# Kernel optimization log

Hardware: AMD Instinct MI355X
Metric: run time of the kernel (lower is better)

## Reference

```python
import jax, jax.numpy as jnp
import numpy as np

B, S, D, H, C = 8, 4096, 1024, 256, 512
INIT_RANGE = 0.01

def setup_inputs() -> dict:
    key = jax.random.key(0)
    ks = jax.random.split(key, 6)
    return {
        "hidden_states": jax.random.normal(ks[0], (B, S, D), dtype=jnp.float32),
        "conditions": jax.random.normal(ks[1], (B, C), dtype=jnp.float32),
        "down_project": jax.random.normal(ks[2], (D, H), dtype=jnp.float32) * INIT_RANGE,
        "down_gamma": jax.random.normal(ks[3], (C, H), dtype=jnp.float32),
        "down_beta": jnp.zeros((C, H), dtype=jnp.float32),
        "up_project": jax.random.normal(ks[4], (H, D), dtype=jnp.float32) * INIT_RANGE,
        "up_gamma": jax.random.normal(ks[5], (C, D), dtype=jnp.float32),
        "up_beta": jnp.zeros((C, D), dtype=jnp.float32),
    }

def reference(hidden_states, conditions, down_project, down_gamma, down_beta,
              up_project, up_gamma, up_beta):
    # per-example modulation coefficients: [B, H] / [B, D]
    dg = conditions @ down_gamma   # [B, H]
    db = conditions @ down_beta    # [B, H]
    ug = conditions @ up_gamma     # [B, D]
    ub = conditions @ up_beta      # [B, D]
    # per-example down weight: W_down * gamma (column scale) + beta (added to every row)
    w_down = down_project[None, :, :] * dg[:, None, :] + db[:, None, :]  # [B, D, H]
    down = jnp.einsum('bsd,bdh->bsh', hidden_states, w_down)             # [B, S, H]
    act = jax.nn.relu(down)
    w_up = up_project[None, :, :] * ug[:, None, :] + ub[:, None, :]      # [B, H, D]
    up = jnp.einsum('bsh,bhd->bsd', act, w_up)                           # [B, S, D]
    # (the original computes self.ln(up) but discards the result)
    return up + hidden_states
```

## Files before the change

### kernel.cpp

```cpp
#include <hip/hip_runtime.h>
#include <hip/hip_bf16.h>

typedef __attribute__((ext_vector_type(4))) float f32x4;
typedef __attribute__((ext_vector_type(8))) short s16x8;
typedef __attribute__((ext_vector_type(8))) unsigned short u16x8;
typedef __attribute__((ext_vector_type(4))) unsigned int u32x4;

#define DEVFN static __device__ __forceinline__

DEVFN unsigned short f2bf(float f) {
  union { float f; unsigned int u; } v; v.f = f;
  unsigned int u = v.u;
  u += 0x7fffu + ((u >> 16) & 1u);
  return (unsigned short)(u >> 16);
}

DEVFN unsigned int cvt_pk(float a, float b) {
  __hip_bfloat162 h = __float22bfloat162_rn(make_float2(a, b));
  union { __hip_bfloat162 h; unsigned int u; } v; v.h = h; return v.u;
}

DEVFN void gl_lds16(const void* g, void* l) {
  __builtin_amdgcn_global_load_lds((__attribute__((address_space(1))) void*)g,
                                   (__attribute__((address_space(3))) void*)l, 16, 0, 0);
}

#define SB() __builtin_amdgcn_sched_barrier(0)
#define VMW(n) asm volatile("s_waitcnt vmcnt(" #n ")" ::: "memory")
#define LGKM0() asm volatile("s_waitcnt lgkmcnt(0)" ::: "memory")
#define BAR() { SB(); __builtin_amdgcn_s_barrier(); SB(); }

#define DG_OFF 0
#define DB_OFF 2048
#define UG_OFF 4096
#define UB_OFF 12288
#define W1_BYTE 81920
#define W2_BYTE 606208

__global__ void prep_kernel(const float* __restrict__ cond,
                            const float* __restrict__ dgm, const float* __restrict__ dbt,
                            const float* __restrict__ ugm, const float* __restrict__ ubt,
                            const float* __restrict__ Wd, const float* __restrict__ Wu,
                            char* __restrict__ ws) {
  __shared__ float lc[4096];
  __shared__ float red[2048];
  const int t = threadIdx.x;

  if (blockIdx.x < 32) {
    const int ks = blockIdx.x;
    const int n = t;
    const float* sp = Wd + (size_t)(ks * 32) * 256 + n;
    unsigned short tmp[32];
#pragma unroll
    for (int kk = 0; kk < 32; ++kk) tmp[kk] = f2bf(sp[(size_t)kk * 256]);
    char* dst = ws + W1_BYTE + (size_t)ks * 16384 + n * 64;
#pragma unroll
    for (int g = 0; g < 4; ++g) {
      u16x8 v;
#pragma unroll
      for (int e = 0; e < 8; ++e) v[e] = tmp[g * 8 + e];
      *(u16x8*)(dst + ((g ^ ((n >> 1) & 3)) << 4)) = v;
    }
    return;
  }
  if (blockIdx.x < 64) {
    int b2 = blockIdx.x - 32;
    int ntile = b2 >> 2, kc = b2 & 3;
    const int n = t >> 1, kh = t & 1;
    const float* sp = Wu + (size_t)(kc * 64 + kh * 32) * 1024 + ntile * 128 + n;
    unsigned short tmp[32];
#pragma unroll
    for (int kk = 0; kk < 32; ++kk) tmp[kk] = f2bf(sp[(size_t)kk * 1024]);
    char* dst = ws + W2_BYTE + (size_t)(ntile * 4 + kc) * 16384 + n * 128;
#pragma unroll
    for (int gi = 0; gi < 4; ++gi) {
      u16x8 v;
#pragma unroll
      for (int e = 0; e < 8; ++e) v[e] = tmp[gi * 8 + e];
      int g = kh * 4 + gi;
      *(u16x8*)(dst + ((g ^ (n & 7)) << 4)) = v;
    }
    return;
  }

  float* coef = (float*)ws;
#pragma unroll
  for (int i = 0; i < 16; ++i) lc[t + i * 256] = cond[t + i * 256];
  __syncthreads();
  const int bid2 = blockIdx.x - 64;
  const int col = bid2 * 16 + (t & 15);
  const int ks = t >> 4;
  const float* src; int ncol, cl;
  if (col < 256)       { src = dgm; ncol = 256;  cl = col; }
  else if (col < 512)  { src = dbt; ncol = 256;  cl = col - 256; }
  else if (col < 1536) { src = ugm; ncol = 1024; cl = col - 512; }
  else                 { src = ubt; ncol = 1024; cl = col - 1536; }
  float acc[8] = {};
  for (int k = ks * 32; k < ks * 32 + 32; ++k) {
    float g = src[(size_t)k * ncol + cl];
#pragma unroll
    for (int b = 0; b < 8; ++b) acc[b] = fmaf(lc[b * 512 + k], g, acc[b]);
  }
#pragma unroll
  for (int b = 0; b < 8; ++b) red[(ks * 16 + (t & 15)) * 8 + b] = acc[b];
  __syncthreads();
  if (t < 128) {
    int c = t >> 3, b = t & 7;
    float s = 0.f;
#pragma unroll
    for (int k2 = 0; k2 < 16; ++k2) s += red[(k2 * 16 + c) * 8 + b];
    int colg = bid2 * 16 + c;
    float* dst; int ncol2, cl2;
    if (colg < 256)       { dst = coef + DG_OFF; ncol2 = 256;  cl2 = colg; }
    else if (colg < 512)  { dst = coef + DB_OFF; ncol2 = 256;  cl2 = colg - 256; }
    else if (colg < 1536) { dst = coef + UG_OFF; ncol2 = 1024; cl2 = colg - 512; }
    else                  { dst = coef + UB_OFF; ncol2 = 1024; cl2 = colg - 1536; }
    dst[b * ncol2 + cl2] = s;
  }
}

__global__ __launch_bounds__(512, 4)
void fused_kernel(const float* __restrict__ X, char* __restrict__ ws,
                  float* __restrict__ out) {
  __shared__ char lds[81920];
  const int tid = threadIdx.x;
  const int lane = tid & 63, lr = lane & 15, lq = lane >> 4;
  const int wave = tid >> 6;
  const int wm = wave >> 2, wn = wave & 3;

  const int raw = blockIdx.x;
  const int m = (raw & 7) * 64 + (raw >> 3);
  const int row0 = m << 6;
  const int b = m >> 6;

  const float* coef = (const float*)ws;
  const char* w1 = ws + W1_BYTE;
  const char* w2 = ws + W2_BYTE;

  const int srow = tid >> 4, sg = tid & 15;
  const float* xsrc = X + (size_t)(row0 + srow) * 1024 + ((sg ^ (srow & 15)) << 2);

  int aoff[2][2][2];
#pragma unroll
  for (int mf = 0; mf < 2; ++mf)
#pragma unroll
    for (int h = 0; h < 2; ++h) {
      int r = wm * 32 + mf * 16 + lr;
      int g0 = h * 8 + lq * 2;
      aoff[mf][h][0] = r * 256 + ((g0 ^ (r & 15)) << 4);
      aoff[mf][h][1] = r * 256 + (((g0 + 1) ^ (r & 15)) << 4);
    }
  int boff[4];
#pragma unroll
  for (int nf = 0; nf < 4; ++nf) {
    int n = wn * 64 + nf * 16 + lr;
    boff[nf] = n * 64 + ((lq ^ ((n >> 1) & 3)) << 4);
  }

  f32x4 acc1[2][4] = {};
  float hacc[2] = {0.f, 0.f};

#define STAGE_X(t)                                                               \
  { char* xb = lds + ((t) & 1) * 16384;                                          \
    gl_lds16(xsrc + (size_t)(t) * 64, xb + tid * 16);                            \
    gl_lds16(xsrc + 32 * 1024 + (size_t)(t) * 64, xb + 8192 + tid * 16); }
#define STAGE_W1(ks)                                                             \
  { char* dst = lds + 32768 + ((ks) % 3) * 16384;                                \
    gl_lds16(w1 + (size_t)(ks) * 16384 + tid * 16, dst + tid * 16);              \
    gl_lds16(w1 + (size_t)(ks) * 16384 + 8192 + tid * 16, dst + 8192 + tid * 16); }

  STAGE_W1(0); STAGE_X(0); STAGE_W1(1);
  VMW(2); BAR();

#pragma unroll
  for (int s = 0; s < 32; ++s) {
    if (s + 2 < 32) STAGE_W1(s + 2);
    if ((s & 1) == 0 && (s >> 1) + 1 < 16) STAGE_X((s >> 1) + 1);
    {
      const char* Xc = lds + ((s >> 1) & 1) * 16384;
      const char* Wb = lds + 32768 + (s % 3) * 16384;
      const int h = s & 1;
      s16x8 afr[2];
#pragma unroll
      for (int mf = 0; mf < 2; ++mf) {
        f32x4 fa0 = *(const f32x4*)(Xc + aoff[mf][h][0]);
        f32x4 fa1 = *(const f32x4*)(Xc + aoff[mf][h][1]);
        if (wn == 0)
          hacc[mf] += fa0[0] + fa0[1] + fa0[2] + fa0[3] +
                      fa1[0] + fa1[1] + fa1[2] + fa1[3];
        union { u32x4 u; s16x8 s_; } cv;
        cv.u[0] = cvt_pk(fa0[0], fa0[1]); cv.u[1] = cvt_pk(fa0[2], fa0[3]);
        cv.u[2] = cvt_pk(fa1[0], fa1[1]); cv.u[3] = cvt_pk(fa1[2], fa1[3]);
        afr[mf] = cv.s_;
      }
      s16x8 bfr[4];
#pragma unroll
      for (int nf = 0; nf < 4; ++nf) bfr[nf] = *(const s16x8*)(Wb + boff[nf]);
#pragma unroll
      for (int mf = 0; mf < 2; ++mf)
#pragma unroll
        for (int nf = 0; nf < 4; ++nf)
          acc1[mf][nf] = __builtin_amdgcn_mfma_f32_16x16x32_bf16(afr[mf], bfr[nf],
                                                                 acc1[mf][nf], 0, 0, 0);
    }
    LGKM0(); SB();
    if (s == 30)            { VMW(0); }
    else if (s == 31)       { }
    else if (s & 1)         { VMW(2); }
    else                    { VMW(4); }
    BAR();
  }

  float* hsumb = (float*)(lds + 32768);
  float* asp   = (float*)(lds + 33024);
  if (wn == 0) {
#pragma unroll
    for (int mf = 0; mf < 2; ++mf) {
      float s = hacc[mf];
      s += __shfl_xor(s, 16); s += __shfl_xor(s, 32);
      if (lq == 0) hsumb[wm * 32 + mf * 16 + lr] = s;
    }
  }
  __syncthreads();

  float dgv[4], dbv[4];
#pragma unroll
  for (int nf = 0; nf < 4; ++nf) {
    int h = wn * 64 + nf * 16 + lr;
    dgv[nf] = coef[DG_OFF + b * 256 + h];
    dbv[nf] = coef[DB_OFF + b * 256 + h];
  }

  float asacc[2][4] = {};
#pragma unroll
  for (int nf = 0; nf < 4; ++nf) {
    int g = nf * 2 + (lr >> 3);
    char* nbase = lds + wn * 8192 + (lr & 7) * 2;
    float dg_ = dgv[nf], db_ = dbv[nf];
#pragma unroll
    for (int mf = 0; mf < 2; ++mf) {
#pragma unroll
      for (int j = 0; j < 4; ++j) {
        int r = wm * 32 + mf * 16 + lq * 4 + j;
        float v = acc1[mf][nf][j] * dg_ + db_ * hsumb[r];
        v = fmaxf(v, 0.f);
        asacc[mf][j] += v;
        *(unsigned short*)(nbase + r * 128 + ((g ^ (r & 7)) << 4)) = f2bf(v);
      }
    }
  }
#pragma unroll
  for (int mf = 0; mf < 2; ++mf)
#pragma unroll
    for (int j = 0; j < 4; ++j) {
      float s = asacc[mf][j];
      s += __shfl_xor(s, 1); s += __shfl_xor(s, 2); s += __shfl_xor(s, 4); s += __shfl_xor(s, 8);
      if (lr == 0) asp[wn * 64 + wm * 32 + mf * 16 + lq * 4 + j] = s;
    }
  __syncthreads();

  float asv[2][4];
#pragma unroll
  for (int mf = 0; mf < 2; ++mf)
#pragma unroll
    for (int j = 0; j < 4; ++j) {
      int r = wm * 32 + mf * 16 + lq * 4 + j;
      asv[mf][j] = asp[r] + asp[64 + r] + asp[128 + r] + asp[192 + r];
    }
  __syncthreads();

  int a2off[2][2], b2off[2][2];
#pragma unroll
  for (int mf = 0; mf < 2; ++mf)
#pragma unroll
    for (int kf = 0; kf < 2; ++kf) {
      int r = wm * 32 + mf * 16 + lr;
      a2off[mf][kf] = r * 128 + (((kf * 4 + lq) ^ (r & 7)) << 4);
    }
#pragma unroll
  for (int nf = 0; nf < 2; ++nf)
#pragma unroll
    for (int kf = 0; kf < 2; ++kf) {
      int nl = wn * 32 + nf * 16 + lr;
      b2off[nf][kf] = nl * 128 + (((kf * 4 + lq) ^ (nl & 7)) << 4);
    }

#define W2B(s) (lds + 32768 + ((s) % 3) * 16384)
#define STAGE_W2(s)                                                              \
  { gl_lds16(w2 + (size_t)(s) * 16384 + tid * 16, W2B(s) + tid * 16);            \
    gl_lds16(w2 + (size_t)(s) * 16384 + 8192 + tid * 16,                         \
             W2B(s) + 8192 + tid * 16); }

  STAGE_W2(0); STAGE_W2(1);
  VMW(2); BAR();

  float ugv[2], ubv[2];
#pragma unroll
  for (int s = 0; s < 32; ++s) {
    const int nt = s >> 2, kc = s & 3;
    f32x4 acc2[2][2];
    if (kc == 0) {
#pragma unroll
      for (int mf = 0; mf < 2; ++mf)
#pragma unroll
        for (int nf = 0; nf < 2; ++nf) acc2[mf][nf] = (f32x4){0.f, 0.f, 0.f, 0.f};
    }
    const char* Wb = W2B(s);
#pragma unroll
    for (int kf = 0; kf < 2; ++kf) {
      s16x8 a2[2], bb[2];
#pragma unroll
      for (int mf = 0; mf < 2; ++mf)
        a2[mf] = *(const s16x8*)(lds + kc * 8192 + a2off[mf][kf]);
#pragma unroll
      for (int nf = 0; nf < 2; ++nf)
        bb[nf] = *(const s16x8*)(Wb + b2off[nf][kf]);
#pragma unroll
      for (int mf = 0; mf < 2; ++mf)
#pragma unroll
        for (int nf = 0; nf < 2; ++nf)
          acc2[mf][nf] = __builtin_amdgcn_mfma_f32_16x16x32_bf16(a2[mf], bb[nf], acc2[mf][nf], 0, 0, 0);
    }
    LGKM0(); SB();

    if (kc == 0) {
#pragma unroll
      for (int nf = 0; nf < 2; ++nf) {
        int d = nt * 128 + wn * 32 + nf * 16 + lr;
        ugv[nf] = coef[UG_OFF + b * 1024 + d];
        ubv[nf] = coef[UB_OFF + b * 1024 + d];
      }
    }
    if (s + 2 < 32) STAGE_W2(s + 2);
    if (kc == 3) {
#pragma unroll
      for (int mf = 0; mf < 2; ++mf)
#pragma unroll
        for (int j = 0; j < 4; ++j) {
          int r = wm * 32 + mf * 16 + lq * 4 + j;
          size_t gbase = (size_t)(row0 + r) * 1024 + nt * 128 + wn * 32;
#pragma unroll
          for (int nf = 0; nf < 2; ++nf) {
            size_t gi = gbase + nf * 16 + lr;
            out[gi] = acc2[mf][nf][j] * ugv[nf] + ubv[nf] * asv[mf][j] + X[gi];
          }
        }
    }
    if (s < 31) {
      if (s + 2 >= 32)  { VMW(0); }
      else if (kc == 3) { VMW(16); }
      else              { VMW(2); }
      BAR();
    }
  }
}

extern "C" void kernel_launch(void* const* d_in, const int* in_sizes, int n_in,
                              void* d_out, int out_size, void* d_ws, size_t ws_size,
                              hipStream_t stream) {
  const float* hidden       = (const float*)d_in[0];
  const float* conditions   = (const float*)d_in[1];
  const float* down_project = (const float*)d_in[2];
  const float* down_gamma   = (const float*)d_in[3];
  const float* down_beta    = (const float*)d_in[4];
  const float* up_project   = (const float*)d_in[5];
  const float* up_gamma     = (const float*)d_in[6];
  const float* up_beta      = (const float*)d_in[7];
  float* out = (float*)d_out;
  char* ws = (char*)d_ws;

  prep_kernel<<<224, 256, 0, stream>>>(conditions, down_gamma, down_beta, up_gamma, up_beta,
                                       down_project, up_project, ws);
  fused_kernel<<<512, 512, 0, stream>>>(hidden, ws, out);
}
```

Measured before the change: 82.04 us.

## Retile first GEMM warps to 4x2 layout and preload up-projection coefficients

The down-projection GEMM's wave tiling changes from 2x4 waves (32 rows x 64 cols each) to 4x2 waves (16 rows x 128 cols each). Each wave now converts one A fragment instead of two, which cuts redundant fp32-to-bf16 conversions and X LDS reads, but it reads eight B fragments per step. The activation write-back and row-sum partials are remapped to the new layout, so the partial sums now combine two entries instead of four. The ug/ub coefficients are also preloaded into registers before the second GEMM instead of being loaded from global memory inside the loop, which costs extra registers.

Result: faster. 80.33 us (-2.1%).

```diff
diff --git a/kernel.cpp b/kernel.cpp
--- a/kernel.cpp
+++ b/kernel.cpp
@@ -126,6 +126,7 @@
   const int tid = threadIdx.x;
   const int lane = tid & 63, lr = lane & 15, lq = lane >> 4;
   const int wave = tid >> 6;
+  const int wm1 = wave >> 1, wn1 = wave & 1;
   const int wm = wave >> 2, wn = wave & 3;
 
   const int raw = blockIdx.x;
@@ -140,25 +141,23 @@
   const int srow = tid >> 4, sg = tid & 15;
   const float* xsrc = X + (size_t)(row0 + srow) * 1024 + ((sg ^ (srow & 15)) << 2);
 
-  int aoff[2][2][2];
-#pragma unroll
-  for (int mf = 0; mf < 2; ++mf)
-#pragma unroll
-    for (int h = 0; h < 2; ++h) {
-      int r = wm * 32 + mf * 16 + lr;
-      int g0 = h * 8 + lq * 2;
-      aoff[mf][h][0] = r * 256 + ((g0 ^ (r & 15)) << 4);
-      aoff[mf][h][1] = r * 256 + (((g0 + 1) ^ (r & 15)) << 4);
-    }
-  int boff[4];
-#pragma unroll
-  for (int nf = 0; nf < 4; ++nf) {
-    int n = wn * 64 + nf * 16 + lr;
+  int aoff1[2][2];
+#pragma unroll
+  for (int h = 0; h < 2; ++h) {
+    int r = wm1 * 16 + lr;
+    int g0 = h * 8 + lq * 2;
+    aoff1[h][0] = r * 256 + ((g0 ^ (r & 15)) << 4);
+    aoff1[h][1] = r * 256 + (((g0 + 1) ^ (r & 15)) << 4);
+  }
+  int boff[8];
+#pragma unroll
+  for (int nf = 0; nf < 8; ++nf) {
+    int n = wn1 * 128 + nf * 16 + lr;
     boff[nf] = n * 64 + ((lq ^ ((n >> 1) & 3)) << 4);
   }
 
-  f32x4 acc1[2][4] = {};
-  float hacc[2] = {0.f, 0.f};
+  f32x4 acc1[8] = {};
+  float hacc = 0.f;
 
 #define STAGE_X(t)                                                               \
   { char* xb = lds + ((t) & 1) * 16384;                                          \
@@ -180,28 +179,22 @@
       const char* Xc = lds + ((s >> 1) & 1) * 16384;
       const char* Wb = lds + 32768 + (s % 3) * 16384;
       const int h = s & 1;
-      s16x8 afr[2];
-#pragma unroll
-      for (int mf = 0; mf < 2; ++mf) {
-        f32x4 fa0 = *(const f32x4*)(Xc + aoff[mf][h][0]);
-        f32x4 fa1 = *(const f32x4*)(Xc + aoff[mf][h][1]);
-        if (wn == 0)
-          hacc[mf] += fa0[0] + fa0[1] + fa0[2] + fa0[3] +
-                      fa1[0] + fa1[1] + fa1[2] + fa1[3];
-        union { u32x4 u; s16x8 s_; } cv;
-        cv.u[0] = cvt_pk(fa0[0], fa0[1]); cv.u[1] = cvt_pk(fa0[2], fa0[3]);
-        cv.u[2] = cvt_pk(fa1[0], fa1[1]); cv.u[3] = cvt_pk(fa1[2], fa1[3]);
-        afr[mf] = cv.s_;
-      }
-      s16x8 bfr[4];
-#pragma unroll
-      for (int nf = 0; nf < 4; ++nf) bfr[nf] = *(const s16x8*)(Wb + boff[nf]);
-#pragma unroll
-      for (int mf = 0; mf < 2; ++mf)
-#pragma unroll
-        for (int nf = 0; nf < 4; ++nf)
-          acc1[mf][nf] = __builtin_amdgcn_mfma_f32_16x16x32_bf16(afr[mf], bfr[nf],
-                                                                 acc1[mf][nf], 0, 0, 0);
+      f32x4 fa0 = *(const f32x4*)(Xc + aoff1[h][0]);
+      f32x4 fa1 = *(const f32x4*)(Xc + aoff1[h][1]);
+      if (wn1 == 0)
+        hacc += fa0[0] + fa0[1] + fa0[2] + fa0[3] +
+                fa1[0] + fa1[1] + fa1[2] + fa1[3];
+      union { u32x4 u; s16x8 s_; } cv;
+      cv.u[0] = cvt_pk(fa0[0], fa0[1]); cv.u[1] = cvt_pk(fa0[2], fa0[3]);
+      cv.u[2] = cvt_pk(fa1[0], fa1[1]); cv.u[3] = cvt_pk(fa1[2], fa1[3]);
+      s16x8 afr = cv.s_;
+      s16x8 bfr[8];
+#pragma unroll
+      for (int nf = 0; nf < 8; ++nf) bfr[nf] = *(const s16x8*)(Wb + boff[nf]);
+#pragma unroll
+      for (int nf = 0; nf < 8; ++nf)
+        acc1[nf] = __builtin_amdgcn_mfma_f32_16x16x32_bf16(afr, bfr[nf],
+                                                           acc1[nf], 0, 0, 0);
     }
     LGKM0(); SB();
     if (s == 30)            { VMW(0); }
@@ -213,50 +206,44 @@
 
   float* hsumb = (float*)(lds + 32768);
   float* asp   = (float*)(lds + 33024);
-  if (wn == 0) {
-#pragma unroll
-    for (int mf = 0; mf < 2; ++mf) {
-      float s = hacc[mf];
-      s += __shfl_xor(s, 16); s += __shfl_xor(s, 32);
-      if (lq == 0) hsumb[wm * 32 + mf * 16 + lr] = s;
-    }
-  }
-  __syncthreads();
-
-  float dgv[4], dbv[4];
-#pragma unroll
-  for (int nf = 0; nf < 4; ++nf) {
-    int h = wn * 64 + nf * 16 + lr;
+  if (wn1 == 0) {
+    float s = hacc;
+    s += __shfl_xor(s, 16); s += __shfl_xor(s, 32);
+    if (lq == 0) hsumb[wm1 * 16 + lr] = s;
+  }
+  __syncthreads();
+
+  float dgv[8], dbv[8];
+#pragma unroll
+  for (int nf = 0; nf < 8; ++nf) {
+    int h = wn1 * 128 + nf * 16 + lr;
     dgv[nf] = coef[DG_OFF + b * 256 + h];
     dbv[nf] = coef[DB_OFF + b * 256 + h];
   }
 
-  float asacc[2][4] = {};
-#pragma unroll
-  for (int nf = 0; nf < 4; ++nf) {
-    int g = nf * 2 + (lr >> 3);
-    char* nbase = lds + wn * 8192 + (lr & 7) * 2;
+  float asacc[4] = {};
+#pragma unroll
+  for (int nf = 0; nf < 8; ++nf) {
+    int hh = wn1 * 128 + nf * 16 + lr;
+    int kc = hh >> 6, kl = hh & 63;
+    int g = kl >> 3;
+    char* nbase = lds + kc * 8192 + (kl & 7) * 2;
     float dg_ = dgv[nf], db_ = dbv[nf];
 #pragma unroll
-    for (int mf = 0; mf < 2; ++mf) {
-#pragma unroll
-      for (int j = 0; j < 4; ++j) {
-        int r = wm * 32 + mf * 16 + lq * 4 + j;
-        float v = acc1[mf][nf][j] * dg_ + db_ * hsumb[r];
-        v = fmaxf(v, 0.f);
-        asacc[mf][j] += v;
-        *(unsigned short*)(nbase + r * 128 + ((g ^ (r & 7)) << 4)) = f2bf(v);
-      }
-    }
-  }
-#pragma unroll
-  for (int mf = 0; mf < 2; ++mf)
-#pragma unroll
     for (int j = 0; j < 4; ++j) {
-      float s = asacc[mf][j];
-      s += __shfl_xor(s, 1); s += __shfl_xor(s, 2); s += __shfl_xor(s, 4); s += __shfl_xor(s, 8);
-      if (lr == 0) asp[wn * 64 + wm * 32 + mf * 16 + lq * 4 + j] = s;
-    }
+      int r = wm1 * 16 + lq * 4 + j;
+      float v = acc1[nf][j] * dg_ + db_ * hsumb[r];
+      v = fmaxf(v, 0.f);
+      asacc[j] += v;
+      *(unsigned short*)(nbase + r * 128 + ((g ^ (r & 7)) << 4)) = f2bf(v);
+    }
+  }
+#pragma unroll
+  for (int j = 0; j < 4; ++j) {
+    float s = asacc[j];
+    s += __shfl_xor(s, 1); s += __shfl_xor(s, 2); s += __shfl_xor(s, 4); s += __shfl_xor(s, 8);
+    if (lr == 0) asp[wn1 * 64 + wm1 * 16 + lq * 4 + j] = s;
+  }
   __syncthreads();
 
   float asv[2][4];
@@ -265,8 +252,22 @@
 #pragma unroll
     for (int j = 0; j < 4; ++j) {
       int r = wm * 32 + mf * 16 + lq * 4 + j;
-      asv[mf][j] = asp[r] + asp[64 + r] + asp[128 + r] + asp[192 + r];
-    }
+      asv[mf][j] = asp[r] + asp[64 + r];
+    }
+  float ugA[8], ubA[8];
+#pragma unroll
+  for (int nt = 0; nt < 8; ++nt) {
+    int d = nt * 128 + wn * 32 + lr;
+    ugA[nt] = coef[UG_OFF + b * 1024 + d];
+    ubA[nt] = coef[UB_OFF + b * 1024 + d];
+  }
+  float ugB[8], ubB[8];
+#pragma unroll
+  for (int nt = 0; nt < 8; ++nt) {
+    int d = nt * 128 + wn * 32 + 16 + lr;
+    ugB[nt] = coef[UG_OFF + b * 1024 + d];
+    ubB[nt] = coef[UB_OFF + b * 1024 + d];
+  }
   __syncthreads();
 
   int a2off[2][2], b2off[2][2];
@@ -294,7 +295,6 @@
   STAGE_W2(0); STAGE_W2(1);
   VMW(2); BAR();
 
-  float ugv[2], ubv[2];
 #pragma unroll
   for (int s = 0; s < 32; ++s) {
     const int nt = s >> 2, kc = s & 3;
@@ -323,14 +323,6 @@
     }
     LGKM0(); SB();
 
-    if (kc == 0) {
-#pragma unroll
-      for (int nf = 0; nf < 2; ++nf) {
-        int d = nt * 128 + wn * 32 + nf * 16 + lr;
-        ugv[nf] = coef[UG_OFF + b * 1024 + d];
-        ubv[nf] = coef[UB_OFF + b * 1024 + d];
-      }
-    }
     if (s + 2 < 32) STAGE_W2(s + 2);
     if (kc == 3) {
 #pragma unroll
@@ -339,11 +331,10 @@
         for (int j = 0; j < 4; ++j) {
           int r = wm * 32 + mf * 16 + lq * 4 + j;
           size_t gbase = (size_t)(row0 + r) * 1024 + nt * 128 + wn * 32;
-#pragma unroll
-          for (int nf = 0; nf < 2; ++nf) {
-            size_t gi = gbase + nf * 16 + lr;
-            out[gi] = acc2[mf][nf][j] * ugv[nf] + ubv[nf] * asv[mf][j] + X[gi];
-          }
+          size_t gi0 = gbase + lr;
+          size_t gi1 = gbase + 16 + lr;
+          out[gi0] = acc2[mf][0][j] * ugA[nt] + ubA[nt] * asv[mf][j] + X[gi0];
+          out[gi1] = acc2[mf][1][j] * ugB[nt] + ubB[nt] * asv[mf][j] + X[gi1];
         }
     }
     if (s < 31) {
```
